# Performance work log

Measured on AMD Instinct MI355X. Metric: run time of the kernel, lower is better.

Reference implementation:

```python
import jax, jax.numpy as jnp
import numpy as np
from jax import lax

T, B, C = 16, 16, 256          # TIMESTEPS, BATCH_SIZE, corr channels
HS, HT = 31, 15                 # search / target feature spatial; VALID corr -> 17x17
OUT = HS - HT + 1               # 17


def setup_inputs() -> dict:
    key = jax.random.key(0)
    k1, k2, k3 = jax.random.split(key, 3)
    s_f = jax.random.normal(k1, (T * B, C, HS, HS), dtype=jnp.float32)
    t_f = jax.random.normal(k2, (B, C, HT, HT), dtype=jnp.float32)
    pos_list = jax.random.randint(k3, (B, T, 2), 0, OUT, dtype=jnp.int32)
    return {"s_f": s_f, "t_f": t_f, "pos_list": pos_list}


def _depthwise_corr(s_b, t_b):
    # s_b: (T, C, 31, 31) search feats for one batch element across timesteps
    # t_b: (C, 15, 15) its target kernel; depthwise cross-correlation per channel
    k = t_b[:, None]  # (C, 1, 15, 15) OIHW with O=C, I=1
    return lax.conv_general_dilated(
        s_b, k, window_strides=(1, 1), padding='VALID',
        dimension_numbers=('NCHW', 'OIHW', 'NCHW'),
        feature_group_count=C)  # (T, C, 17, 17)


def reference(s_f, t_f, pos_list):
    # Correlation_func: torch loops over T doing grouped conv2d; fused here.
    s = s_f.reshape(T, B, C, HS, HS).transpose(1, 0, 2, 3, 4)  # (B, T, C, 31, 31)
    corr = jax.vmap(_depthwise_corr)(s, t_f)                   # (B, T, C, 17, 17)
    # forward(): corr_feat.reshape(T,B,256,17,17).permute(1,0,3,4,2) -> (B,T,17,17,C)
    feat = corr.transpose(0, 1, 3, 4, 2)
    # Chiose_RoW: nested per-element gather -> single advanced-index gather
    bi = jnp.arange(B)[:, None]   # (B, 1)
    ti = jnp.arange(T)[None, :]   # (1, T)
    masks_feat = feat[bi, ti, pos_list[..., 0], pos_list[..., 1]]  # (B, T, C)
    return corr, masks_feat
```

## Files before the change

kernel.cpp:

```cpp
#include <hip/hip_runtime.h>
#include <stdint.h>

#define TT 16
#define BB 16
#define CC 256
#define HS 31
#define HT 15
#define OUTW 17
#define NCH 15
#define NCHAN (BB*TT*CC)
#define CORR_ELEMS ((size_t)NCHAN*OUTW*OUTW)

typedef _Float16 h2_t __attribute__((ext_vector_type(2)));

__device__ __forceinline__ unsigned packh2(float a, float b) {
    return __builtin_bit_cast(unsigned, __builtin_amdgcn_cvt_pkrtz(a, b));
}
__device__ __forceinline__ float fdot2f(unsigned a, unsigned b, float c) {
    return __builtin_amdgcn_fdot2(__builtin_bit_cast(h2_t, a),
                                  __builtin_bit_cast(h2_t, b), c, false);
}

__device__ __forceinline__ int s_index(int ch) {
    int bt = ch >> 8, c = ch & 255;
    int b = bt >> 4, t = bt & 15;
    return (t * BB + b) * CC + c;
}

__global__ __launch_bounds__(256, 4)
void corr_kernel(const float* __restrict__ s_f, const float* __restrict__ t_f,
                 float* __restrict__ corr)
{
    __shared__ __align__(16) unsigned s_u32[NCH][HS][16];
    __shared__ __align__(16) unsigned w_u32[NCH][HT][8];

    const int tid = threadIdx.x;
    const int ch_base = blockIdx.x * NCH;

    {
        const int jcol = tid & 15;
        const int r0   = tid >> 4;
        const int x0   = 2 * jcol;
        const bool hasb  = (jcol < 15);
        const int  r1    = r0 + 16;
        const bool hasr1 = (r1 < HS);
        const int c0 = (((jcol >> 2) ^ (r0 & 3)) << 2) | (jcol & 3);
        const int c1 = (((jcol >> 2) ^ (r1 & 3)) << 2) | (jcol & 3);
#pragma unroll
        for (int j = 0; j < NCH; ++j) {
            int ch = ch_base + j; if (ch >= NCHAN) ch = NCHAN - 1;
            const float* src = s_f + (size_t)s_index(ch) * (HS * HS);
            float a0 = src[r0 * HS + x0];
            float b0 = hasb ? src[r0 * HS + x0 + 1] : 0.0f;
            float a1 = hasr1 ? src[r1 * HS + x0] : 0.0f;
            float b1 = (hasr1 && hasb) ? src[r1 * HS + x0 + 1] : 0.0f;
            s_u32[j][r0][c0] = packh2(a0, b0);
            if (hasr1) s_u32[j][r1][c1] = packh2(a1, b1);
        }
    }

    {
        const int j    = tid >> 4;
        const int lane = tid & 15;
        if (j < NCH) {
            int ch = ch_base + j; if (ch >= NCHAN) ch = NCHAN - 1;
            int bt = ch >> 8, c = ch & 255, b = bt >> 4;
            const float* wsrc = t_f + (size_t)(b * CC + c) * (HT * HT);
#pragma unroll
            for (int q0 = 0; q0 < 8; ++q0) {
                int q = q0 * 16 + lane;
                if (q < HT * 8) {
                    int ky = q >> 3, p = q & 7;
                    float a  = wsrc[ky * HT + 2 * p];
                    float bb = (p < 7) ? wsrc[ky * HT + 2 * p + 1] : 0.0f;
                    w_u32[j][ky][p] = packh2(a, bb);
                }
            }
        }
    }

    __syncthreads();

    const int c_sub = tid / OUTW;
    const int oy    = tid - c_sub * OUTW;
    const int ch    = ch_base + c_sub;
    if (c_sub >= NCH || ch >= NCHAN) return;

    float acc[OUTW];
#pragma unroll
    for (int m = 0; m < OUTW; ++m) acc[m] = 0.0f;

#pragma unroll 1
    for (int ky = 0; ky < HT; ++ky) {
        const int y  = oy + ky;
        const int sw = y & 3;

        unsigned wp[8], wo[8];
        {
            const uint4* rp = (const uint4*)(&w_u32[c_sub][ky][0]);
            uint4 w0 = rp[0], w1 = rp[1];
            wp[0] = w0.x; wp[1] = w0.y; wp[2] = w0.z; wp[3] = w0.w;
            wp[4] = w1.x; wp[5] = w1.y; wp[6] = w1.z; wp[7] = w1.w;
            wo[0] = __builtin_amdgcn_alignbit(wp[0], 0u, 16);
#pragma unroll
            for (int r = 1; r < 8; ++r)
                wo[r] = __builtin_amdgcn_alignbit(wp[r], wp[r - 1], 16);
        }

        const uint4* srow = (const uint4*)(&s_u32[c_sub][y][0]);
#pragma unroll
        for (int u = 0; u < 4; ++u) {
            uint4 d = srow[u ^ sw];
            unsigned spc[4] = {d.x, d.y, d.z, d.w};
#pragma unroll
            for (int q = 0; q < 4; ++q) {
                const int p = 4 * u + q;
#pragma unroll
                for (int j = (p > 8 ? p - 8 : 0); j <= (p < 7 ? p : 7); ++j)
                    acc[2 * (p - j)] = fdot2f(spc[q], wp[j], acc[2 * (p - j)]);
#pragma unroll
                for (int r = (p > 7 ? p - 7 : 0); r <= (p < 7 ? p : 7); ++r)
                    acc[2 * (p - r) + 1] = fdot2f(spc[q], wo[r], acc[2 * (p - r) + 1]);
            }
        }
    }

    size_t base = (size_t)ch * (OUTW * OUTW) + (size_t)oy * OUTW;
#pragma unroll
    for (int m = 0; m < OUTW; ++m) corr[base + m] = acc[m];
}

__global__ void masks_kernel(const float* __restrict__ corr,
                             const int* __restrict__ pos,
                             float* __restrict__ masks)
{
    int gid = blockIdx.x * 256 + threadIdx.x;
    if (gid >= NCHAN) return;
    int bt = gid >> 8;
    int b  = bt >> 4;
    int t  = bt & 15;
    int p0 = pos[(b * TT + t) * 2 + 0];
    int p1 = pos[(b * TT + t) * 2 + 1];
    masks[gid] = corr[(size_t)gid * (OUTW * OUTW) + p0 * OUTW + p1];
}

extern "C" void kernel_launch(void* const* d_in, const int* in_sizes, int n_in,
                              void* d_out, int out_size, void* d_ws, size_t ws_size,
                              hipStream_t stream)
{
    const float* s_f = (const float*)d_in[0];
    const float* t_f = (const float*)d_in[1];
    const int*   pos = (const int*)d_in[2];
    float* corr  = (float*)d_out;
    float* masks = corr + CORR_ELEMS;

    int nblocks = (NCHAN + NCH - 1) / NCH;
    corr_kernel<<<nblocks, 256, 0, stream>>>(s_f, t_f, corr);
    masks_kernel<<<NCHAN / 256, 256, 0, stream>>>(corr, pos, masks);
}
```

Baseline: 151.0 us.

## Compute depthwise correlation with MFMA f16 matrix cores per wavefront

Replaces the scalar fdot2 sliding-window correlation with a per-wave MFMA formulation. Each wave handles one channel, stages the search image (plus a one-pixel-shifted copy) and the kernel in LDS as f16, and runs 16x16x32 MFMAs per output column. Partial products are written back to LDS as f16, then summed along diagonals with shuffles. This adds many partial-sum round trips through LDS and f16 accumulation, which risks precision loss, and relies on wave-synchronous LDS access with no explicit barriers.

```diff
diff --git a/kernel.cpp b/kernel.cpp
--- a/kernel.cpp
+++ b/kernel.cpp
@@ -7,19 +7,13 @@
 #define HS 31
 #define HT 15
 #define OUTW 17
-#define NCH 15
 #define NCHAN (BB*TT*CC)
 #define CORR_ELEMS ((size_t)NCHAN*OUTW*OUTW)
+#define SW 48
+#define NW 4
 
-typedef _Float16 h2_t __attribute__((ext_vector_type(2)));
-
-__device__ __forceinline__ unsigned packh2(float a, float b) {
-    return __builtin_bit_cast(unsigned, __builtin_amdgcn_cvt_pkrtz(a, b));
-}
-__device__ __forceinline__ float fdot2f(unsigned a, unsigned b, float c) {
-    return __builtin_amdgcn_fdot2(__builtin_bit_cast(h2_t, a),
-                                  __builtin_bit_cast(h2_t, b), c, false);
-}
+typedef _Float16 half8 __attribute__((ext_vector_type(8)));
+typedef float    f32x4 __attribute__((ext_vector_type(4)));
 
 __device__ __forceinline__ int s_index(int ch) {
     int bt = ch >> 8, c = ch & 255;
@@ -27,107 +21,108 @@
     return (t * BB + b) * CC + c;
 }
 
+__device__ __forceinline__ unsigned packh2(float a, float b) {
+    return __builtin_bit_cast(unsigned, __builtin_amdgcn_cvt_pkrtz(a, b));
+}
+
+__device__ __forceinline__ half8 ldsA(const _Float16* p) {
+    const unsigned* u = (const unsigned*)p;
+    union { unsigned x[4]; half8 h; } r;
+    r.x[0] = u[0]; r.x[1] = u[1]; r.x[2] = u[2]; r.x[3] = u[3];
+    return r.h;
+}
+
 __global__ __launch_bounds__(256, 4)
-void corr_kernel(const float* __restrict__ s_f, const float* __restrict__ t_f,
-                 float* __restrict__ corr)
+void corr_mfma(const float* __restrict__ s_f, const float* __restrict__ t_f,
+               float* __restrict__ corr)
 {
-    __shared__ __align__(16) unsigned s_u32[NCH][HS][16];
-    __shared__ __align__(16) unsigned w_u32[NCH][HT][8];
+    __shared__ __align__(16) _Float16 s2[NW][2][32][SW];
+    __shared__ __align__(16) _Float16 wl[NW][16][32];
+    __shared__ __align__(16) _Float16 r2[NW][16][32];
 
-    const int tid = threadIdx.x;
-    const int ch_base = blockIdx.x * NCH;
+    const int tid  = threadIdx.x;
+    const int w    = tid >> 6;
+    const int lane = tid & 63;
+    const int ch   = blockIdx.x * NW + w;
 
     {
-        const int jcol = tid & 15;
-        const int r0   = tid >> 4;
-        const int x0   = 2 * jcol;
-        const bool hasb  = (jcol < 15);
-        const int  r1    = r0 + 16;
-        const bool hasr1 = (r1 < HS);
-        const int c0 = (((jcol >> 2) ^ (r0 & 3)) << 2) | (jcol & 3);
-        const int c1 = (((jcol >> 2) ^ (r1 & 3)) << 2) | (jcol & 3);
+        uint4 z{0, 0, 0, 0};
+        uint4* p = (uint4*)&s2[w][0][0][0];
 #pragma unroll
-        for (int j = 0; j < NCH; ++j) {
-            int ch = ch_base + j; if (ch >= NCHAN) ch = NCHAN - 1;
-            const float* src = s_f + (size_t)s_index(ch) * (HS * HS);
-            float a0 = src[r0 * HS + x0];
-            float b0 = hasb ? src[r0 * HS + x0 + 1] : 0.0f;
-            float a1 = hasr1 ? src[r1 * HS + x0] : 0.0f;
-            float b1 = (hasr1 && hasb) ? src[r1 * HS + x0 + 1] : 0.0f;
-            s_u32[j][r0][c0] = packh2(a0, b0);
-            if (hasr1) s_u32[j][r1][c1] = packh2(a1, b1);
+        for (int i = 0; i < 6; ++i) p[i * 64 + lane] = z;
+        ((uint4*)&wl[w][0][0])[lane] = z;
+    }
+
+    {
+        const float* src = s_f + (size_t)s_index(ch) * (HS * HS);
+#pragma unroll
+        for (int i = 0; i < 16; ++i) {
+            int e = i * 64 + lane;
+            if (e < HS * HS) {
+                int y = e / HS;
+                int x = e - y * HS;
+                _Float16 v = (_Float16)src[e];
+                s2[w][0][y][x] = v;
+                if (x > 0) s2[w][1][y][x - 1] = v;
+            }
         }
     }
 
     {
-        const int j    = tid >> 4;
-        const int lane = tid & 15;
-        if (j < NCH) {
-            int ch = ch_base + j; if (ch >= NCHAN) ch = NCHAN - 1;
-            int bt = ch >> 8, c = ch & 255, b = bt >> 4;
-            const float* wsrc = t_f + (size_t)(b * CC + c) * (HT * HT);
+        const int bt = ch >> 8, c = ch & 255, b = bt >> 4;
+        const float* wsrc = t_f + (size_t)(b * CC + c) * (HT * HT);
 #pragma unroll
-            for (int q0 = 0; q0 < 8; ++q0) {
-                int q = q0 * 16 + lane;
-                if (q < HT * 8) {
-                    int ky = q >> 3, p = q & 7;
-                    float a  = wsrc[ky * HT + 2 * p];
-                    float bb = (p < 7) ? wsrc[ky * HT + 2 * p + 1] : 0.0f;
-                    w_u32[j][ky][p] = packh2(a, bb);
-                }
+        for (int i = 0; i < 4; ++i) {
+            int e = i * 64 + lane;
+            if (e < HT * HT) {
+                int ky = e / HT;
+                int kx = e - ky * HT;
+                wl[w][ky][kx] = (_Float16)wsrc[e];
             }
         }
     }
 
-    __syncthreads();
+    const int r = lane & 15;
+    const int q = lane >> 4;
+    half8 bfrag = *(const half8*)&wl[w][r][8 * q];
 
-    const int c_sub = tid / OUTW;
-    const int oy    = tid - c_sub * OUTW;
-    const int ch    = ch_base + c_sub;
-    if (c_sub >= NCH || ch >= NCHAN) return;
+    const int  h   = lane / 17;
+    const int  oy  = lane - 17 * h;
+    const bool act = (h < 3);
+    const _Float16* r2h  = &r2[w][0][0];
+    const int       rbase = oy + (5 * h) * 33;
+    float* outp = corr + (size_t)ch * (OUTW * OUTW) + oy * OUTW;
 
-    float acc[OUTW];
-#pragma unroll
-    for (int m = 0; m < OUTW; ++m) acc[m] = 0.0f;
+    const f32x4 zero{0.f, 0.f, 0.f, 0.f};
 
-#pragma unroll 1
-    for (int ky = 0; ky < HT; ++ky) {
-        const int y  = oy + ky;
-        const int sw = y & 3;
+    for (int ox = 0; ox < OUTW; ++ox) {
+        const int c  = ox & 1;
+        const int pb = (ox - c) + 8 * q;
 
-        unsigned wp[8], wo[8];
+        half8 a0 = ldsA(&s2[w][c][r][pb]);
+        half8 a1 = ldsA(&s2[w][c][r + 16][pb]);
+
+        f32x4 c0 = __builtin_amdgcn_mfma_f32_16x16x32_f16(a0, bfrag, zero, 0, 0, 0);
+        f32x4 c1 = __builtin_amdgcn_mfma_f32_16x16x32_f16(a1, bfrag, zero, 0, 0, 0);
+
         {
-            const uint4* rp = (const uint4*)(&w_u32[c_sub][ky][0]);
-            uint4 w0 = rp[0], w1 = rp[1];
-            wp[0] = w0.x; wp[1] = w0.y; wp[2] = w0.z; wp[3] = w0.w;
-            wp[4] = w1.x; wp[5] = w1.y; wp[6] = w1.z; wp[7] = w1.w;
-            wo[0] = __builtin_amdgcn_alignbit(wp[0], 0u, 16);
-#pragma unroll
-            for (int r = 1; r < 8; ++r)
-                wo[r] = __builtin_amdgcn_alignbit(wp[r], wp[r - 1], 16);
+            uint2 v0{packh2(c0[0], c0[1]), packh2(c0[2], c0[3])};
+            uint2 v1{packh2(c1[0], c1[1]), packh2(c1[2], c1[3])};
+            *(uint2*)&r2[w][r][4 * q]      = v0;
+            *(uint2*)&r2[w][r][4 * q + 16] = v1;
         }
 
-        const uint4* srow = (const uint4*)(&s_u32[c_sub][y][0]);
+        if (act) {
+            _Float16 acc = (_Float16)0;
 #pragma unroll
-        for (int u = 0; u < 4; ++u) {
-            uint4 d = srow[u ^ sw];
-            unsigned spc[4] = {d.x, d.y, d.z, d.w};
-#pragma unroll
-            for (int q = 0; q < 4; ++q) {
-                const int p = 4 * u + q;
-#pragma unroll
-                for (int j = (p > 8 ? p - 8 : 0); j <= (p < 7 ? p : 7); ++j)
-                    acc[2 * (p - j)] = fdot2f(spc[q], wp[j], acc[2 * (p - j)]);
-#pragma unroll
-                for (int r = (p > 7 ? p - 7 : 0); r <= (p < 7 ? p : 7); ++r)
-                    acc[2 * (p - r) + 1] = fdot2f(spc[q], wo[r], acc[2 * (p - r) + 1]);
-            }
+            for (int k = 0; k < 5; ++k)
+                acc += r2h[rbase + k * 33];
+            float p  = (float)acc;
+            float p1 = __shfl(p, (lane + 17) & 63);
+            float p2 = __shfl(p, (lane + 34) & 63);
+            if (h == 0) outp[ox] = p + p1 + p2;
         }
     }
-
-    size_t base = (size_t)ch * (OUTW * OUTW) + (size_t)oy * OUTW;
-#pragma unroll
-    for (int m = 0; m < OUTW; ++m) corr[base + m] = acc[m];
 }
 
 __global__ void masks_kernel(const float* __restrict__ corr,
@@ -154,7 +149,6 @@
     float* corr  = (float*)d_out;
     float* masks = corr + CORR_ELEMS;
 
-    int nblocks = (NCHAN + NCH - 1) / NCH;
-    corr_kernel<<<nblocks, 256, 0, stream>>>(s_f, t_f, corr);
+    corr_mfma<<<NCHAN / NW, 256, 0, stream>>>(s_f, t_f, corr);
     masks_kernel<<<NCHAN / 256, 256, 0, stream>>>(corr, pos, masks);
 }
```

Result: slower. 288.4 us (+91.0%).

## Pad LDS rows instead of XOR swizzle and fully unroll ky loop

Applied to the files above, without the earlier changes.

Replaces the XOR-swizzled 16-word shared-memory rows with 17-word padded rows and scalar 32-bit loads, and fully unrolls the kernel-row loop. Channels per block drop from 15 to 14, and the weight staging becomes a flat strided loop. The goal is to avoid LDS bank conflicts with simpler addressing and to let the compiler schedule across ky iterations. In exchange it issues 16 scalar LDS reads per row instead of 4 vector reads, uses more registers, and covers fewer channels per block, which means more blocks.

```diff
diff --git a/kernel.cpp b/kernel.cpp
--- a/kernel.cpp
+++ b/kernel.cpp
@@ -7,9 +7,12 @@
 #define HS 31
 #define HT 15
 #define OUTW 17
-#define NCH 15
+#define NCH 14
 #define NCHAN (BB*TT*CC)
 #define CORR_ELEMS ((size_t)NCHAN*OUTW*OUTW)
+#define SROW 17
+#define SCH  545
+#define WCH  120
 
 typedef _Float16 h2_t __attribute__((ext_vector_type(2)));
 
@@ -31,8 +34,8 @@
 void corr_kernel(const float* __restrict__ s_f, const float* __restrict__ t_f,
                  float* __restrict__ corr)
 {
-    __shared__ __align__(16) unsigned s_u32[NCH][HS][16];
-    __shared__ __align__(16) unsigned w_u32[NCH][HT][8];
+    __shared__ unsigned s_lds[NCH * SCH];
+    __shared__ unsigned w_lds[NCH * WCH];
 
     const int tid = threadIdx.x;
     const int ch_base = blockIdx.x * NCH;
@@ -43,86 +46,75 @@
         const int x0   = 2 * jcol;
         const bool hasb  = (jcol < 15);
         const int  r1    = r0 + 16;
-        const bool hasr1 = (r1 < HS);
-        const int c0 = (((jcol >> 2) ^ (r0 & 3)) << 2) | (jcol & 3);
-        const int c1 = (((jcol >> 2) ^ (r1 & 3)) << 2) | (jcol & 3);
+        const bool hasr1 = (r1 <= 30);
 #pragma unroll
         for (int j = 0; j < NCH; ++j) {
             int ch = ch_base + j; if (ch >= NCHAN) ch = NCHAN - 1;
             const float* src = s_f + (size_t)s_index(ch) * (HS * HS);
             float a0 = src[r0 * HS + x0];
             float b0 = hasb ? src[r0 * HS + x0 + 1] : 0.0f;
-            float a1 = hasr1 ? src[r1 * HS + x0] : 0.0f;
-            float b1 = (hasr1 && hasb) ? src[r1 * HS + x0 + 1] : 0.0f;
-            s_u32[j][r0][c0] = packh2(a0, b0);
-            if (hasr1) s_u32[j][r1][c1] = packh2(a1, b1);
+            s_lds[j * SCH + r0 * SROW + jcol] = packh2(a0, b0);
+            if (hasr1) {
+                float a1 = src[r1 * HS + x0];
+                float b1 = hasb ? src[r1 * HS + x0 + 1] : 0.0f;
+                s_lds[j * SCH + r1 * SROW + jcol] = packh2(a1, b1);
+            }
         }
     }
 
-    {
-        const int j    = tid >> 4;
-        const int lane = tid & 15;
-        if (j < NCH) {
-            int ch = ch_base + j; if (ch >= NCHAN) ch = NCHAN - 1;
-            int bt = ch >> 8, c = ch & 255, b = bt >> 4;
-            const float* wsrc = t_f + (size_t)(b * CC + c) * (HT * HT);
-#pragma unroll
-            for (int q0 = 0; q0 < 8; ++q0) {
-                int q = q0 * 16 + lane;
-                if (q < HT * 8) {
-                    int ky = q >> 3, p = q & 7;
-                    float a  = wsrc[ky * HT + 2 * p];
-                    float bb = (p < 7) ? wsrc[ky * HT + 2 * p + 1] : 0.0f;
-                    w_u32[j][ky][p] = packh2(a, bb);
-                }
-            }
-        }
+    for (int idx = tid; idx < NCH * HT * 8; idx += 256) {
+        int j   = idx / (HT * 8);
+        int rem = idx - j * (HT * 8);
+        int ky  = rem >> 3;
+        int p   = rem & 7;
+        int ch  = ch_base + j; if (ch >= NCHAN) ch = NCHAN - 1;
+        int bt = ch >> 8, c = ch & 255, b = bt >> 4;
+        const float* wsrc = t_f + (size_t)(b * CC + c) * (HT * HT) + ky * HT;
+        float a  = wsrc[2 * p];
+        float bb = (p < 7) ? wsrc[2 * p + 1] : 0.0f;
+        w_lds[j * WCH + ky * 8 + p] = packh2(a, bb);
     }
 
     __syncthreads();
 
     const int c_sub = tid / OUTW;
     const int oy    = tid - c_sub * OUTW;
-    const int ch    = ch_base + c_sub;
-    if (c_sub >= NCH || ch >= NCHAN) return;
+    if (c_sub >= NCH) return;
+    const int ch = ch_base + c_sub;
+    if (ch >= NCHAN) return;
+
+    const unsigned* sbase = &s_lds[c_sub * SCH + oy * SROW];
+    const unsigned* wbase = &w_lds[c_sub * WCH];
 
     float acc[OUTW];
 #pragma unroll
     for (int m = 0; m < OUTW; ++m) acc[m] = 0.0f;
 
-#pragma unroll 1
+#pragma unroll
     for (int ky = 0; ky < HT; ++ky) {
-        const int y  = oy + ky;
-        const int sw = y & 3;
+        unsigned sp[16];
+#pragma unroll
+        for (int u = 0; u < 16; ++u) sp[u] = sbase[ky * SROW + u];
 
-        unsigned wp[8], wo[8];
-        {
-            const uint4* rp = (const uint4*)(&w_u32[c_sub][ky][0]);
-            uint4 w0 = rp[0], w1 = rp[1];
-            wp[0] = w0.x; wp[1] = w0.y; wp[2] = w0.z; wp[3] = w0.w;
-            wp[4] = w1.x; wp[5] = w1.y; wp[6] = w1.z; wp[7] = w1.w;
-            wo[0] = __builtin_amdgcn_alignbit(wp[0], 0u, 16);
+        uint4 w0 = *(const uint4*)(wbase + ky * 8);
+        uint4 w1 = *(const uint4*)(wbase + ky * 8 + 4);
+        unsigned wp[8] = {w0.x, w0.y, w0.z, w0.w, w1.x, w1.y, w1.z, w1.w};
+        unsigned wo[8];
+        wo[0] = wp[0] << 16;
 #pragma unroll
-            for (int r = 1; r < 8; ++r)
-                wo[r] = __builtin_amdgcn_alignbit(wp[r], wp[r - 1], 16);
-        }
+        for (int r = 1; r < 8; ++r)
+            wo[r] = __builtin_amdgcn_alignbit(wp[r], wp[r - 1], 16);
 
-        const uint4* srow = (const uint4*)(&s_u32[c_sub][y][0]);
 #pragma unroll
-        for (int u = 0; u < 4; ++u) {
-            uint4 d = srow[u ^ sw];
-            unsigned spc[4] = {d.x, d.y, d.z, d.w};
+        for (int e = 0; e < 9; ++e)
 #pragma unroll
-            for (int q = 0; q < 4; ++q) {
-                const int p = 4 * u + q;
+            for (int jj = 0; jj < 8; ++jj)
+                acc[2 * e] = fdot2f(sp[e + jj], wp[jj], acc[2 * e]);
 #pragma unroll
-                for (int j = (p > 8 ? p - 8 : 0); j <= (p < 7 ? p : 7); ++j)
-                    acc[2 * (p - j)] = fdot2f(spc[q], wp[j], acc[2 * (p - j)]);
+        for (int o = 0; o < 8; ++o)
 #pragma unroll
-                for (int r = (p > 7 ? p - 7 : 0); r <= (p < 7 ? p : 7); ++r)
-                    acc[2 * (p - r) + 1] = fdot2f(spc[q], wo[r], acc[2 * (p - r) + 1]);
-            }
-        }
+            for (int r = 0; r < 8; ++r)
+                acc[2 * o + 1] = fdot2f(sp[o + r], wo[r], acc[2 * o + 1]);
     }
 
     size_t base = (size_t)ch * (OUTW * OUTW) + (size_t)oy * OUTW;
```

After: 167.8 us. +11.1%, slower.
